# Performance work log

Hardware: AMD Instinct MI355X
Metric: run time of the kernel (lower is better)

## Reference

```python
import jax, jax.numpy as jnp
import numpy as np

B, T, E, H = 2, 2048, 1024, 16
HS = E // H  # head size 64


def setup_inputs() -> dict:
    key = jax.random.key(0)
    ks = jax.random.split(key, 6)
    s = 0.02
    return {
        "x": jax.random.normal(ks[0], (B, T, E), dtype=jnp.float32),
        "Wq": jax.random.normal(ks[1], (E, E), dtype=jnp.float32) * s,
        "Wk": jax.random.normal(ks[2], (E, E), dtype=jnp.float32) * s,
        "Wv": jax.random.normal(ks[3], (E, E), dtype=jnp.float32) * s,
        "Wp": jax.random.normal(ks[4], (E, E), dtype=jnp.float32) * s,
        "bp": jax.random.normal(ks[5], (E,), dtype=jnp.float32) * s,
    }


def reference(x, Wq, Wk, Wv, Wp, bp):
    b, t, e = x.shape
    # per-head projections (concatenated heads == single E->E matmul, reshaped)
    def heads(w):
        return jnp.einsum('bte,ef->btf', x, w).reshape(b, t, H, HS).transpose(0, 2, 1, 3)
    q, k, v = heads(Wq), heads(Wk), heads(Wv)  # [B,H,T,HS]
    # NOTE: original scales by full embed dim E, not head_size
    scores = jnp.einsum('bhqd,bhkd->bhqk', q, k) * (e ** -0.5)
    causal = jnp.tril(jnp.ones((t, t), dtype=bool))
    scores = jnp.where(causal, scores, -jnp.inf)
    probs = jax.nn.softmax(scores, axis=-1)
    # dropout is identity in eval mode
    out = jnp.einsum('bhqk,bhkd->bhqd', probs, v)  # [B,H,T,HS]
    out = out.transpose(0, 2, 1, 3).reshape(b, t, e)
    return jnp.einsum('bte,ef->btf', out, Wp) + bp
```

## Files before the change

kernel.cpp:

```cpp
#include <hip/hip_runtime.h>
#include <math.h>

typedef __bf16 bf16x8 __attribute__((ext_vector_type(8)));
typedef __bf16 bf16x4 __attribute__((ext_vector_type(4)));
typedef float f32x4 __attribute__((ext_vector_type(4)));

constexpr int Bb = 2, Tt = 2048, Ee = 1024, Hh = 16, Hs = 64;
constexpr int Mm = Bb * Tt;

__device__ inline unsigned short f2bf(float f) {
    union { float f; unsigned u; } c; c.f = f;
    unsigned u = c.u;
    u += 0x7FFFu + ((u >> 16) & 1u);
    return (unsigned short)(u >> 16);
}

__device__ inline void gl2lds16(const void* g, void* l) {
    __builtin_amdgcn_global_load_lds(
        (const __attribute__((address_space(1))) void*)g,
        (__attribute__((address_space(3))) void*)l, 16, 0, 0);
}

__global__ __launch_bounds__(256) void conv_x(const float* __restrict__ x,
                                              unsigned short* __restrict__ xb) {
    int gid = blockIdx.x * 256 + threadIdx.x;
    float4 v = ((const float4*)x)[gid];
    ushort4 o;
    o.x = f2bf(v.x); o.y = f2bf(v.y); o.z = f2bf(v.z); o.w = f2bf(v.w);
    ((ushort4*)xb)[gid] = o;
}

__global__ __launch_bounds__(256) void transpose_w4(const float* __restrict__ Wq,
                                                    const float* __restrict__ Wk,
                                                    const float* __restrict__ Wv,
                                                    const float* __restrict__ Wp,
                                                    unsigned short* __restrict__ wt3,
                                                    unsigned short* __restrict__ wpt) {
    __shared__ unsigned short t[64][68];
    const float* W = (blockIdx.z == 0) ? Wq : (blockIdx.z == 1) ? Wk
                    : (blockIdx.z == 2) ? Wv : Wp;
    unsigned short* dst = (blockIdx.z < 3) ? wt3 + (size_t)blockIdx.z * 1024 * 1024 : wpt;
    const int tid = threadIdx.x;
    const int k0 = blockIdx.x * 64, n0 = blockIdx.y * 64;
#pragma unroll
    for (int j = 0; j < 4; j++) {
        int row = (tid >> 4) + j * 16;
        int c4 = (tid & 15) * 4;
        float4 v = *(const float4*)&W[(size_t)(k0 + row) * 1024 + n0 + c4];
        t[row][c4 + 0] = f2bf(v.x); t[row][c4 + 1] = f2bf(v.y);
        t[row][c4 + 2] = f2bf(v.z); t[row][c4 + 3] = f2bf(v.w);
    }
    __syncthreads();
#pragma unroll
    for (int j = 0; j < 16; j++) {
        int flat = j * 256 + tid;
        int orow = flat >> 6, ocol = flat & 63;
        dst[(size_t)(n0 + orow) * 1024 + k0 + ocol] = t[ocol][orow];
    }
}

__device__ inline void gemm_mainloop(const unsigned short* __restrict__ A,
                                     const unsigned short* __restrict__ Bt,
                                     unsigned short* As, unsigned short* Bs,
                                     int bm, int bn, int tid, f32x4 (&acc)[4][4]) {
    const int lane = tid & 63, w = tid >> 6;
    const int quad = lane >> 4, cl = lane & 15;
    const int wm = (w >> 1) * 64, wn = (w & 1) * 64;

    auto stage = [&](int k0) {
#pragma unroll
        for (int i = 0; i < 2; i++) {
            int L = tid + i * 256;
            int r = L >> 2;
            int kc = (L & 3) ^ (r & 3);
            gl2lds16(A + (size_t)(bm + r) * 1024 + k0 + kc * 8, &As[L * 8]);
        }
#pragma unroll
        for (int i = 0; i < 2; i++) {
            int L = tid + i * 256;
            int r = L >> 2;
            int kc = (L & 3) ^ (r & 3);
            gl2lds16(Bt + (size_t)(bn + r) * 1024 + k0 + kc * 8, &Bs[L * 8]);
        }
    };

    stage(0);
    __syncthreads();
    for (int k0 = 0;;) {
        bf16x8 af[4], bfr[4];
#pragma unroll
        for (int mt = 0; mt < 4; mt++) {
            int r = wm + mt * 16 + cl;
            af[mt] = *(const bf16x8*)&As[(r * 4 + (quad ^ (r & 3))) * 8];
            int rb = wn + mt * 16 + cl;
            bfr[mt] = *(const bf16x8*)&Bs[(rb * 4 + (quad ^ (rb & 3))) * 8];
        }
#pragma unroll
        for (int mt = 0; mt < 4; mt++)
#pragma unroll
            for (int nt = 0; nt < 4; nt++)
                acc[mt][nt] = __builtin_amdgcn_mfma_f32_16x16x32_bf16(
                    af[mt], bfr[nt], acc[mt][nt], 0, 0, 0);
        k0 += 32;
        if (k0 >= 1024) break;
        __syncthreads();
        stage(k0);
        __syncthreads();
    }
}

__global__ __launch_bounds__(256, 2) void gemm_qkv(const unsigned short* __restrict__ A,
                                                   const unsigned short* __restrict__ Bt,
                                                   unsigned short* __restrict__ qb,
                                                   unsigned short* __restrict__ kb,
                                                   unsigned short* __restrict__ vtb) {
    __shared__ unsigned short As[128 * 32];
    __shared__ unsigned short Bs[128 * 32];
    const int tid = threadIdx.x;
    const int bm = blockIdx.y * 128;
    const int bn = blockIdx.x * 128;
    f32x4 acc[4][4] = {};
    gemm_mainloop(A, Bt, As, Bs, bm, bn, tid, acc);

    const int lane = tid & 63, w = tid >> 6;
    const int quad = lane >> 4, cl = lane & 15;
    const int wm = (w >> 1) * 64, wn = (w & 1) * 64;
    const int region = bn >> 10;

    if (region < 2) {
        unsigned short* dst = region ? kb : qb;
        const float qs = region ? 1.0f : 0.045084220027780107f;
#pragma unroll
        for (int mt = 0; mt < 4; mt++)
#pragma unroll
            for (int nt = 0; nt < 4; nt++)
#pragma unroll
                for (int rg = 0; rg < 4; rg++) {
                    int m = bm + wm + mt * 16 + quad * 4 + rg;
                    int nn = (bn + wn + nt * 16 + cl) & 1023;
                    int b = m >> 11, t = m & 2047, h = nn >> 6, hs = nn & 63;
                    dst[((size_t)(b * 16 + h) * 2048 + t) * 64 + hs] =
                        f2bf(acc[mt][nt][rg] * qs);
                }
    } else {
#pragma unroll
        for (int mt = 0; mt < 4; mt++) {
            int m0 = bm + wm + mt * 16 + quad * 4;
            int b = m0 >> 11, t0 = m0 & 2047;
#pragma unroll
            for (int nt = 0; nt < 4; nt++) {
                int nn = (bn + wn + nt * 16 + cl) & 1023;
                int h = nn >> 6, hs = nn & 63;
                ushort4 pk;
                pk.x = f2bf(acc[mt][nt][0]); pk.y = f2bf(acc[mt][nt][1]);
                pk.z = f2bf(acc[mt][nt][2]); pk.w = f2bf(acc[mt][nt][3]);
                *(ushort4*)&vtb[((size_t)(b * 16 + h) * 64 + hs) * 2048 + t0] = pk;
            }
        }
    }
}

__global__ __launch_bounds__(256, 2) void gemm_out(const unsigned short* __restrict__ A,
                                                   const unsigned short* __restrict__ Bt,
                                                   const float* __restrict__ bias,
                                                   float* __restrict__ out) {
    __shared__ unsigned short As[128 * 32];
    __shared__ unsigned short Bs[128 * 32];
    const int tid = threadIdx.x;
    const int bm = blockIdx.y * 128;
    const int bn = blockIdx.x * 128;
    f32x4 acc[4][4] = {};
    gemm_mainloop(A, Bt, As, Bs, bm, bn, tid, acc);

    const int lane = tid & 63, w = tid >> 6;
    const int quad = lane >> 4, cl = lane & 15;
    const int wm = (w >> 1) * 64, wn = (w & 1) * 64;
#pragma unroll
    for (int mt = 0; mt < 4; mt++)
#pragma unroll
        for (int nt = 0; nt < 4; nt++)
#pragma unroll
            for (int rg = 0; rg < 4; rg++) {
                int m = bm + wm + mt * 16 + quad * 4 + rg;
                int n = bn + wn + nt * 16 + cl;
                out[(size_t)m * 1024 + n] = acc[mt][nt][rg] + bias[n];
            }
}

__global__ __launch_bounds__(256, 4) void attn_mfma(const unsigned short* __restrict__ qg,
                                                    const unsigned short* __restrict__ kg,
                                                    const unsigned short* __restrict__ vtg,
                                                    unsigned short* __restrict__ og) {
    __shared__ unsigned short Qlds[64 * 64];
    __shared__ unsigned short Klds[64 * 64];
    __shared__ unsigned short Vlds[64 * 64];
    const int tid = threadIdx.x;
    const int bh = blockIdx.x;
    const int qt = 31 - (int)blockIdx.y;
    const int lane = tid & 63, w = tid >> 6;
    const int quad = lane >> 4, cl = lane & 15;
    const int qbase = qt * 64;
    const unsigned short* qB = qg + (size_t)bh * 2048 * 64;
    const unsigned short* kB = kg + (size_t)bh * 2048 * 64;
    const unsigned short* vB = vtg + (size_t)bh * 64 * 2048;

    auto stageKV = [&](int kt) {
#pragma unroll
        for (int i = 0; i < 2; i++) {
            int L = tid + i * 256;
            int r = L >> 3;
            int kc = (L & 7) ^ (r & 7);
            gl2lds16(kB + (size_t)(kt * 64 + r) * 64 + kc * 8, &Klds[L * 8]);
            gl2lds16(vB + (size_t)r * 2048 + kt * 64 + kc * 8, &Vlds[L * 8]);
        }
    };

#pragma unroll
    for (int i = 0; i < 2; i++) {
        int L = tid + i * 256;
        int r = L >> 3;
        int kc = (L & 7) ^ (r & 7);
        gl2lds16(qB + (size_t)(qbase + r) * 64 + kc * 8, &Qlds[L * 8]);
    }
    stageKV(0);
    __syncthreads();

    bf16x8 qf[2];
#pragma unroll
    for (int kf = 0; kf < 2; kf++) {
        int r = w * 16 + cl, cc = kf * 4 + quad;
        qf[kf] = *(const bf16x8*)&Qlds[(r * 8 + (cc ^ (r & 7))) * 8];
    }

    bf16x8 ones;
#pragma unroll
    for (int j = 0; j < 8; j++) ones[j] = (__bf16)1.0f;

    f32x4 oacc[4] = {};
    f32x4 lacc = {};
    unsigned short* Pw = &Qlds[w * 1024];
    const int thr = w * 16 + cl - quad * 4;

    for (int kt = 0; kt <= qt; kt++) {
        const bool diag = (kt == qt);
        f32x4 sac[4] = {};
#pragma unroll
        for (int kf = 0; kf < 2; kf++)
#pragma unroll
            for (int mt = 0; mt < 4; mt++) {
                int r = mt * 16 + cl, cc = kf * 4 + quad;
                bf16x8 kf8 = *(const bf16x8*)&Klds[(r * 8 + (cc ^ (r & 7))) * 8];
                sac[mt] = __builtin_amdgcn_mfma_f32_16x16x32_bf16(
                    kf8, qf[kf], sac[mt], 0, 0, 0);
            }
        if (!diag) {
#pragma unroll
            for (int mt = 0; mt < 4; mt++) {
                bf16x4 p4;
#pragma unroll
                for (int rg = 0; rg < 4; rg++) p4[rg] = (__bf16)exp2f(sac[mt][rg]);
                int c = mt * 2 + (quad >> 1);
                *(bf16x4*)&Pw[(cl * 8 + (c ^ (cl & 7))) * 8 + (quad & 1) * 4] = p4;
            }
        } else {
#pragma unroll
            for (int mt = 0; mt < 4; mt++) {
                bf16x4 p4;
#pragma unroll
                for (int rg = 0; rg < 4; rg++) {
                    float p = (mt * 16 + rg <= thr) ? exp2f(sac[mt][rg]) : 0.0f;
                    p4[rg] = (__bf16)p;
                }
                int c = mt * 2 + (quad >> 1);
                *(bf16x4*)&Pw[(cl * 8 + (c ^ (cl & 7))) * 8 + (quad & 1) * 4] = p4;
            }
        }
#pragma unroll
        for (int kf = 0; kf < 2; kf++) {
            int ccp = kf * 4 + quad;
            bf16x8 pf = *(const bf16x8*)&Pw[(cl * 8 + (ccp ^ (cl & 7))) * 8];
            lacc = __builtin_amdgcn_mfma_f32_16x16x32_bf16(pf, ones, lacc, 0, 0, 0);
#pragma unroll
            for (int nt = 0; nt < 4; nt++) {
                int r = nt * 16 + cl, cc = kf * 4 + quad;
                bf16x8 vf = *(const bf16x8*)&Vlds[(r * 8 + (cc ^ (r & 7))) * 8];
                oacc[nt] = __builtin_amdgcn_mfma_f32_16x16x32_bf16(
                    pf, vf, oacc[nt], 0, 0, 0);
            }
        }
        __syncthreads();
        if (kt < qt) stageKV(kt + 1);
        __syncthreads();
    }

    const int b = bh >> 4, h = bh & 15;
#pragma unroll
    for (int rg = 0; rg < 4; rg++) {
        float inv = 1.0f / lacc[rg];
        int t = qbase + w * 16 + quad * 4 + rg;
#pragma unroll
        for (int nt = 0; nt < 4; nt++) {
            int hs = nt * 16 + cl;
            og[((size_t)(b * 2048 + t)) * 1024 + h * 64 + hs] = f2bf(oacc[nt][rg] * inv);
        }
    }
}

extern "C" void kernel_launch(void* const* d_in, const int* in_sizes, int n_in,
                              void* d_out, int out_size, void* d_ws, size_t ws_size,
                              hipStream_t stream) {
    const float* x = (const float*)d_in[0];
    const float* Wq = (const float*)d_in[1];
    const float* Wk = (const float*)d_in[2];
    const float* Wv = (const float*)d_in[3];
    const float* Wp = (const float*)d_in[4];
    const float* bp = (const float*)d_in[5];
    float* out = (float*)d_out;

    unsigned short* xb = (unsigned short*)d_ws;
    unsigned short* wt3 = xb + (size_t)Mm * Ee;
    unsigned short* wpt = wt3 + (size_t)3 * Ee * Ee;
    unsigned short* qb = wpt + (size_t)Ee * Ee;
    unsigned short* kb = qb + (size_t)Mm * Ee;
    unsigned short* vtb = kb + (size_t)Mm * Ee;
    unsigned short* ab = vtb + (size_t)Mm * Ee;

    conv_x<<<dim3(Mm * Ee / 4 / 256), dim3(256), 0, stream>>>(x, xb);
    transpose_w4<<<dim3(16, 16, 4), dim3(256), 0, stream>>>(Wq, Wk, Wv, Wp, wt3, wpt);

    gemm_qkv<<<dim3(24, 32), dim3(256), 0, stream>>>(xb, wt3, qb, kb, vtb);
    attn_mfma<<<dim3(32, 32), dim3(256), 0, stream>>>(qb, kb, vtb, ab);
    gemm_out<<<dim3(8, 32), dim3(256), 0, stream>>>(ab, wpt, bp, out);
}
```

Measured before the change: 183.6 us.

## Merge prep kernels, enlarge attention query tile with double-buffered KV, shrink output GEMM tile

```diff
diff --git a/kernel.cpp b/kernel.cpp
--- a/kernel.cpp
+++ b/kernel.cpp
@@ -21,26 +21,31 @@
         (__attribute__((address_space(3))) void*)l, 16, 0, 0);
 }
 
-__global__ __launch_bounds__(256) void conv_x(const float* __restrict__ x,
-                                              unsigned short* __restrict__ xb) {
-    int gid = blockIdx.x * 256 + threadIdx.x;
-    float4 v = ((const float4*)x)[gid];
-    ushort4 o;
-    o.x = f2bf(v.x); o.y = f2bf(v.y); o.z = f2bf(v.z); o.w = f2bf(v.w);
-    ((ushort4*)xb)[gid] = o;
-}
-
-__global__ __launch_bounds__(256) void transpose_w4(const float* __restrict__ Wq,
-                                                    const float* __restrict__ Wk,
-                                                    const float* __restrict__ Wv,
-                                                    const float* __restrict__ Wp,
-                                                    unsigned short* __restrict__ wt3,
-                                                    unsigned short* __restrict__ wpt) {
+__global__ __launch_bounds__(256) void prep(const float* __restrict__ x,
+                                            const float* __restrict__ Wq,
+                                            const float* __restrict__ Wk,
+                                            const float* __restrict__ Wv,
+                                            const float* __restrict__ Wp,
+                                            unsigned short* __restrict__ xb,
+                                            unsigned short* __restrict__ wt3,
+                                            unsigned short* __restrict__ wpt) {
+    const int tid = threadIdx.x;
+    if (blockIdx.z == 4) {
+        int flat = (blockIdx.y * 16 + blockIdx.x) * 256 + tid;
+#pragma unroll
+        for (int i = 0; i < 16; i++) {
+            int gid = flat + i * 65536;
+            float4 v = ((const float4*)x)[gid];
+            ushort4 o;
+            o.x = f2bf(v.x); o.y = f2bf(v.y); o.z = f2bf(v.z); o.w = f2bf(v.w);
+            ((ushort4*)xb)[gid] = o;
+        }
+        return;
+    }
     __shared__ unsigned short t[64][68];
     const float* W = (blockIdx.z == 0) ? Wq : (blockIdx.z == 1) ? Wk
                     : (blockIdx.z == 2) ? Wv : Wp;
     unsigned short* dst = (blockIdx.z < 3) ? wt3 + (size_t)blockIdx.z * 1024 * 1024 : wpt;
-    const int tid = threadIdx.x;
     const int k0 = blockIdx.x * 64, n0 = blockIdx.y * 64;
 #pragma unroll
     for (int j = 0; j < 4; j++) {
@@ -160,23 +165,65 @@
     }
 }
 
-__global__ __launch_bounds__(256, 2) void gemm_out(const unsigned short* __restrict__ A,
+__global__ __launch_bounds__(256, 4) void gemm_out(const unsigned short* __restrict__ A,
                                                    const unsigned short* __restrict__ Bt,
                                                    const float* __restrict__ bias,
                                                    float* __restrict__ out) {
-    __shared__ unsigned short As[128 * 32];
+    __shared__ unsigned short As[64 * 32];
     __shared__ unsigned short Bs[128 * 32];
     const int tid = threadIdx.x;
-    const int bm = blockIdx.y * 128;
+    const int bm = blockIdx.y * 64;
     const int bn = blockIdx.x * 128;
-    f32x4 acc[4][4] = {};
-    gemm_mainloop(A, Bt, As, Bs, bm, bn, tid, acc);
-
     const int lane = tid & 63, w = tid >> 6;
     const int quad = lane >> 4, cl = lane & 15;
-    const int wm = (w >> 1) * 64, wn = (w & 1) * 64;
-#pragma unroll
-    for (int mt = 0; mt < 4; mt++)
+    const int wm = (w >> 1) * 32, wn = (w & 1) * 64;
+    f32x4 acc[2][4] = {};
+
+    auto stage = [&](int k0) {
+        {
+            int L = tid;
+            int r = L >> 2;
+            int kc = (L & 3) ^ (r & 3);
+            gl2lds16(A + (size_t)(bm + r) * 1024 + k0 + kc * 8, &As[L * 8]);
+        }
+#pragma unroll
+        for (int i = 0; i < 2; i++) {
+            int L = tid + i * 256;
+            int r = L >> 2;
+            int kc = (L & 3) ^ (r & 3);
+            gl2lds16(Bt + (size_t)(bn + r) * 1024 + k0 + kc * 8, &Bs[L * 8]);
+        }
+    };
+
+    stage(0);
+    __syncthreads();
+    for (int k0 = 0;;) {
+        bf16x8 af[2], bfr[4];
+#pragma unroll
+        for (int mt = 0; mt < 2; mt++) {
+            int r = wm + mt * 16 + cl;
+            af[mt] = *(const bf16x8*)&As[(r * 4 + (quad ^ (r & 3))) * 8];
+        }
+#pragma unroll
+        for (int nt = 0; nt < 4; nt++) {
+            int rb = wn + nt * 16 + cl;
+            bfr[nt] = *(const bf16x8*)&Bs[(rb * 4 + (quad ^ (rb & 3))) * 8];
+        }
+#pragma unroll
+        for (int mt = 0; mt < 2; mt++)
+#pragma unroll
+            for (int nt = 0; nt < 4; nt++)
+                acc[mt][nt] = __builtin_amdgcn_mfma_f32_16x16x32_bf16(
+                    af[mt], bfr[nt], acc[mt][nt], 0, 0, 0);
+        k0 += 32;
+        if (k0 >= 1024) break;
+        __syncthreads();
+        stage(k0);
+        __syncthreads();
+    }
+
+#pragma unroll
+    for (int mt = 0; mt < 2; mt++)
 #pragma unroll
         for (int nt = 0; nt < 4; nt++)
 #pragma unroll
@@ -187,123 +234,139 @@
             }
 }
 
-__global__ __launch_bounds__(256, 4) void attn_mfma(const unsigned short* __restrict__ qg,
+__global__ __launch_bounds__(256, 3) void attn_mfma(const unsigned short* __restrict__ qg,
                                                     const unsigned short* __restrict__ kg,
                                                     const unsigned short* __restrict__ vtg,
                                                     unsigned short* __restrict__ og) {
-    __shared__ unsigned short Qlds[64 * 64];
-    __shared__ unsigned short Klds[64 * 64];
-    __shared__ unsigned short Vlds[64 * 64];
+    __shared__ unsigned short Qlds[128 * 64];
+    __shared__ unsigned short Klds[2][64 * 64];
+    __shared__ unsigned short Vlds[2][64 * 64];
     const int tid = threadIdx.x;
-    const int bh = blockIdx.x;
-    const int qt = 31 - (int)blockIdx.y;
+    const int idx = blockIdx.x;
+    const int bh = idx & 31;
+    const int j = 15 - (idx >> 5);
     const int lane = tid & 63, w = tid >> 6;
     const int quad = lane >> 4, cl = lane & 15;
-    const int qbase = qt * 64;
+    const int qbase = j * 128;
+    const int wq0 = w * 32;
     const unsigned short* qB = qg + (size_t)bh * 2048 * 64;
     const unsigned short* kB = kg + (size_t)bh * 2048 * 64;
     const unsigned short* vB = vtg + (size_t)bh * 64 * 2048;
 
-    auto stageKV = [&](int kt) {
+    auto stageKV = [&](int kt, int buf) {
 #pragma unroll
         for (int i = 0; i < 2; i++) {
             int L = tid + i * 256;
             int r = L >> 3;
             int kc = (L & 7) ^ (r & 7);
-            gl2lds16(kB + (size_t)(kt * 64 + r) * 64 + kc * 8, &Klds[L * 8]);
-            gl2lds16(vB + (size_t)r * 2048 + kt * 64 + kc * 8, &Vlds[L * 8]);
+            gl2lds16(kB + (size_t)(kt * 64 + r) * 64 + kc * 8, &Klds[buf][L * 8]);
+            gl2lds16(vB + (size_t)r * 2048 + kt * 64 + kc * 8, &Vlds[buf][L * 8]);
         }
     };
 
 #pragma unroll
-    for (int i = 0; i < 2; i++) {
+    for (int i = 0; i < 4; i++) {
         int L = tid + i * 256;
         int r = L >> 3;
         int kc = (L & 7) ^ (r & 7);
         gl2lds16(qB + (size_t)(qbase + r) * 64 + kc * 8, &Qlds[L * 8]);
     }
-    stageKV(0);
+    stageKV(0, 0);
     __syncthreads();
 
-    bf16x8 qf[2];
-#pragma unroll
-    for (int kf = 0; kf < 2; kf++) {
-        int r = w * 16 + cl, cc = kf * 4 + quad;
-        qf[kf] = *(const bf16x8*)&Qlds[(r * 8 + (cc ^ (r & 7))) * 8];
-    }
+    bf16x8 qf[2][2];
+#pragma unroll
+    for (int nt2 = 0; nt2 < 2; nt2++)
+#pragma unroll
+        for (int kf = 0; kf < 2; kf++) {
+            int r = wq0 + nt2 * 16 + cl, cc = kf * 4 + quad;
+            qf[nt2][kf] = *(const bf16x8*)&Qlds[(r * 8 + (cc ^ (r & 7))) * 8];
+        }
 
     bf16x8 ones;
 #pragma unroll
-    for (int j = 0; j < 8; j++) ones[j] = (__bf16)1.0f;
-
-    f32x4 oacc[4] = {};
-    f32x4 lacc = {};
-    unsigned short* Pw = &Qlds[w * 1024];
-    const int thr = w * 16 + cl - quad * 4;
-
-    for (int kt = 0; kt <= qt; kt++) {
-        const bool diag = (kt == qt);
-        f32x4 sac[4] = {};
-#pragma unroll
-        for (int kf = 0; kf < 2; kf++)
-#pragma unroll
-            for (int mt = 0; mt < 4; mt++) {
-                int r = mt * 16 + cl, cc = kf * 4 + quad;
-                bf16x8 kf8 = *(const bf16x8*)&Klds[(r * 8 + (cc ^ (r & 7))) * 8];
-                sac[mt] = __builtin_amdgcn_mfma_f32_16x16x32_bf16(
-                    kf8, qf[kf], sac[mt], 0, 0, 0);
+    for (int i = 0; i < 8; i++) ones[i] = (__bf16)1.0f;
+
+    f32x4 oacc[2][4] = {};
+    f32x4 lacc[2] = {};
+    unsigned short* Pw = &Qlds[w * 2048];
+    const int ntiles = 2 * j + 2;
+    const int dkt = 2 * j + (w >> 1);
+    const int qloc0 = (w & 1) * 32;
+
+    for (int kt = 0; kt < ntiles; kt++) {
+        const int buf = kt & 1;
+        if (kt + 1 < ntiles) stageKV(kt + 1, buf ^ 1);
+        if (kt <= dkt) {
+            const bool diag = (kt == dkt);
+            f32x4 sac[4][2] = {};
+#pragma unroll
+            for (int kf = 0; kf < 2; kf++)
+#pragma unroll
+                for (int mt = 0; mt < 4; mt++) {
+                    int r = mt * 16 + cl, cc = kf * 4 + quad;
+                    bf16x8 kf8 = *(const bf16x8*)&Klds[buf][(r * 8 + (cc ^ (r & 7))) * 8];
+#pragma unroll
+                    for (int nt2 = 0; nt2 < 2; nt2++)
+                        sac[mt][nt2] = __builtin_amdgcn_mfma_f32_16x16x32_bf16(
+                            kf8, qf[nt2][kf], sac[mt][nt2], 0, 0, 0);
+                }
+#pragma unroll
+            for (int mt = 0; mt < 4; mt++)
+#pragma unroll
+                for (int nt2 = 0; nt2 < 2; nt2++) {
+                    bf16x4 p4;
+#pragma unroll
+                    for (int rg = 0; rg < 4; rg++) {
+                        float p = exp2f(sac[mt][nt2][rg]);
+                        if (diag && (mt * 16 + quad * 4 + rg > qloc0 + nt2 * 16 + cl))
+                            p = 0.0f;
+                        p4[rg] = (__bf16)p;
+                    }
+                    int r2 = nt2 * 16 + cl;
+                    int c = mt * 2 + (quad >> 1);
+                    *(bf16x4*)&Pw[(r2 * 8 + (c ^ (r2 & 7))) * 8 + (quad & 1) * 4] = p4;
+                }
+#pragma unroll
+            for (int ks = 0; ks < 2; ks++) {
+                bf16x8 pf[2];
+#pragma unroll
+                for (int mt2 = 0; mt2 < 2; mt2++) {
+                    int r2 = mt2 * 16 + cl, cc = ks * 4 + quad;
+                    pf[mt2] = *(const bf16x8*)&Pw[(r2 * 8 + (cc ^ (r2 & 7))) * 8];
+                }
+#pragma unroll
+                for (int mt2 = 0; mt2 < 2; mt2++)
+                    lacc[mt2] = __builtin_amdgcn_mfma_f32_16x16x32_bf16(
+                        pf[mt2], ones, lacc[mt2], 0, 0, 0);
+#pragma unroll
+                for (int nt = 0; nt < 4; nt++) {
+                    int r = nt * 16 + cl, cc = ks * 4 + quad;
+                    bf16x8 vf = *(const bf16x8*)&Vlds[buf][(r * 8 + (cc ^ (r & 7))) * 8];
+#pragma unroll
+                    for (int mt2 = 0; mt2 < 2; mt2++)
+                        oacc[mt2][nt] = __builtin_amdgcn_mfma_f32_16x16x32_bf16(
+                            pf[mt2], vf, oacc[mt2][nt], 0, 0, 0);
+                }
             }
-        if (!diag) {
-#pragma unroll
-            for (int mt = 0; mt < 4; mt++) {
-                bf16x4 p4;
-#pragma unroll
-                for (int rg = 0; rg < 4; rg++) p4[rg] = (__bf16)exp2f(sac[mt][rg]);
-                int c = mt * 2 + (quad >> 1);
-                *(bf16x4*)&Pw[(cl * 8 + (c ^ (cl & 7))) * 8 + (quad & 1) * 4] = p4;
+        }
+        __syncthreads();
+    }
+
+    const int b = bh >> 4, h = bh & 15;
+#pragma unroll
+    for (int mt2 = 0; mt2 < 2; mt2++)
+#pragma unroll
+        for (int rg = 0; rg < 4; rg++) {
+            float inv = 1.0f / lacc[mt2][rg];
+            int t = qbase + wq0 + mt2 * 16 + quad * 4 + rg;
+#pragma unroll
+            for (int nt = 0; nt < 4; nt++) {
+                int hs = nt * 16 + cl;
+                og[((size_t)(b * 2048 + t)) * 1024 + h * 64 + hs] =
+                    f2bf(oacc[mt2][nt][rg] * inv);
             }
-        } else {
-#pragma unroll
-            for (int mt = 0; mt < 4; mt++) {
-                bf16x4 p4;
-#pragma unroll
-                for (int rg = 0; rg < 4; rg++) {
-                    float p = (mt * 16 + rg <= thr) ? exp2f(sac[mt][rg]) : 0.0f;
-                    p4[rg] = (__bf16)p;
-                }
-                int c = mt * 2 + (quad >> 1);
-                *(bf16x4*)&Pw[(cl * 8 + (c ^ (cl & 7))) * 8 + (quad & 1) * 4] = p4;
-            }
-        }
-#pragma unroll
-        for (int kf = 0; kf < 2; kf++) {
-            int ccp = kf * 4 + quad;
-            bf16x8 pf = *(const bf16x8*)&Pw[(cl * 8 + (ccp ^ (cl & 7))) * 8];
-            lacc = __builtin_amdgcn_mfma_f32_16x16x32_bf16(pf, ones, lacc, 0, 0, 0);
-#pragma unroll
-            for (int nt = 0; nt < 4; nt++) {
-                int r = nt * 16 + cl, cc = kf * 4 + quad;
-                bf16x8 vf = *(const bf16x8*)&Vlds[(r * 8 + (cc ^ (r & 7))) * 8];
-                oacc[nt] = __builtin_amdgcn_mfma_f32_16x16x32_bf16(
-                    pf, vf, oacc[nt], 0, 0, 0);
-            }
-        }
-        __syncthreads();
-        if (kt < qt) stageKV(kt + 1);
-        __syncthreads();
-    }
-
-    const int b = bh >> 4, h = bh & 15;
-#pragma unroll
-    for (int rg = 0; rg < 4; rg++) {
-        float inv = 1.0f / lacc[rg];
-        int t = qbase + w * 16 + quad * 4 + rg;
-#pragma unroll
-        for (int nt = 0; nt < 4; nt++) {
-            int hs = nt * 16 + cl;
-            og[((size_t)(b * 2048 + t)) * 1024 + h * 64 + hs] = f2bf(oacc[nt][rg] * inv);
-        }
-    }
+        }
 }
 
 extern "C" void kernel_launch(void* const* d_in, const int* in_sizes, int n_in,
@@ -325,10 +388,8 @@
     unsigned short* vtb = kb + (size_t)Mm * Ee;
     unsigned short* ab = vtb + (size_t)Mm * Ee;
 
-    conv_x<<<dim3(Mm * Ee / 4 / 256), dim3(256), 0, stream>>>(x, xb);
-    transpose_w4<<<dim3(16, 16, 4), dim3(256), 0, stream>>>(Wq, Wk, Wv, Wp, wt3, wpt);
-
+    prep<<<dim3(16, 16, 5), dim3(256), 0, stream>>>(x, Wq, Wk, Wv, Wp, xb, wt3, wpt);
     gemm_qkv<<<dim3(24, 32), dim3(256), 0, stream>>>(xb, wt3, qb, kb, vtb);
-    attn_mfma<<<dim3(32, 32), dim3(256), 0, stream>>>(qb, kb, vtb, ab);
-    gemm_out<<<dim3(8, 32), dim3(256), 0, stream>>>(ab, wpt, bp, out);
-}
+    attn_mfma<<<dim3(512), dim3(256), 0, stream>>>(qb, kb, vtb, ab);
+    gemm_out<<<dim3(8, 64), dim3(256), 0, stream>>>(ab, wpt, bp, out);
+}
```

Measured after the change: 181.2 us. About the same (-1.3%).
